# Optimization experiments

Measured on AMD Instinct MI355X. Metric: run time of the kernel, lower is better.

The kernel has to match this reference:

```python
import jax, jax.numpy as jnp
import numpy as np

B_, L, DM, DS, DC, EX = 8, 1024, 256, 16, 4, 2
DI = EX * DM            # d_inner = 512
DTR = max(DM // 16, 1)  # dt_rank = 16


def setup_inputs() -> dict:
    key = jax.random.key(0)
    ks = jax.random.split(key, 16)
    s = lambda i, shape, sc=0.05: jax.random.normal(ks[i], shape, dtype=jnp.float32) * sc
    return {
        "state": jax.random.normal(ks[0], (B_, L, DM), dtype=jnp.float32),
        "in_proj_w": s(1, (2 * DI, DM)),
        "conv_w": s(2, (DI, DC)),
        "conv_b": s(3, (DI,)),
        "x_proj_w": s(4, (DTR + 2 * DS, DI)),
        "dt_proj_w": s(5, (DI, DTR), 0.5),
        "dt_proj_b": s(6, (DI,)),
        "A_log": jnp.log(jnp.broadcast_to(jnp.arange(1, DS + 1, dtype=jnp.float32), (DI, DS))),
        "D": jnp.ones((DI,), jnp.float32),
        "out_proj_w": s(7, (DM, DI)),
        "w1": s(8, (DM, 256)), "b1": jnp.zeros((256,), jnp.float32),
        "w2": s(9, (256, 128)), "b2": jnp.zeros((128,), jnp.float32),
        "w3": s(10, (128, 1)), "b3": jnp.zeros((1,), jnp.float32),
    }


def reference(state, in_proj_w, conv_w, conv_b, x_proj_w, dt_proj_w, dt_proj_b,
              A_log, D, out_proj_w, w1, b1, w2, b2, w3, b3):
    # --- Mamba block ---
    xz = jnp.einsum('bld,ed->ble', state, in_proj_w)      # (B, L, 2*DI)
    x, z = jnp.split(xz, 2, axis=-1)
    # causal depthwise conv1d (kernel DC), small unrolled loop over taps
    xp = jnp.pad(x, ((0, 0), (DC - 1, 0), (0, 0)))
    xc = sum(xp[:, k:k + L, :] * conv_w[:, k] for k in range(DC)) + conv_b
    x = jax.nn.silu(xc)                                   # (B, L, DI)
    x_dbl = jnp.einsum('bld,ed->ble', x, x_proj_w)        # (B, L, DTR+2*DS)
    dtr, Bm, Cm = jnp.split(x_dbl, [DTR, DTR + DS], axis=-1)
    dt = jax.nn.softplus(jnp.einsum('blr,dr->bld', dtr, dt_proj_w) + dt_proj_b)
    A = -jnp.exp(A_log)                                   # (DI, DS)
    dA = jnp.exp(dt[..., None] * A)                       # (B, L, DI, DS)
    dBu = dt[..., None] * Bm[:, :, None, :] * x[..., None]

    def step(h, inp):
        dA_t, dBu_t, C_t = inp
        h = dA_t * h + dBu_t                              # (B, DI, DS)
        return h, jnp.einsum('bdn,bn->bd', h, C_t)

    h0 = jnp.zeros((x.shape[0], DI, DS), x.dtype)
    _, ys = jax.lax.scan(step, h0, (jnp.swapaxes(dA, 0, 1),
                                    jnp.swapaxes(dBu, 0, 1),
                                    jnp.swapaxes(Cm, 0, 1)))
    y = jnp.swapaxes(ys, 0, 1) + x * D                    # (B, L, DI)
    y = y * jax.nn.silu(z)
    out = jnp.einsum('bld,ed->ble', y, out_proj_w)        # (B, L, DM)
    # --- squeeze is a no-op for these shapes; MLP value head ---
    h1 = jax.nn.relu(out @ w1 + b1)
    h2 = jax.nn.relu(h1 @ w2 + b2)
    return h2 @ w3 + b3                                   # (B, L, 1)
```

## Files before the change

### kernel.cpp

```cpp
#include <hip/hip_runtime.h>
#include <cstdint>
#include <cmath>

#define B_   8
#define L_   1024
#define DM_  256
#define DS_  16
#define DC_  4
#define DI_  512
#define DTR_ 16
#define M_   (B_*L_)
#define NCH  64
#define CH   16

using half8 = __attribute__((ext_vector_type(8))) _Float16;
using half4 = __attribute__((ext_vector_type(4))) _Float16;
using f32x4 = __attribute__((ext_vector_type(4))) float;

template<bool F32>
__device__ __forceinline__ half8 load_h8(const void* base, size_t off)
{
    if constexpr (F32) {
        const float* p = (const float*)base + off;
        const float4 a = *reinterpret_cast<const float4*>(p);
        const float4 b = *reinterpret_cast<const float4*>(p + 4);
        half8 h;
        h[0] = (_Float16)a.x; h[1] = (_Float16)a.y;
        h[2] = (_Float16)a.z; h[3] = (_Float16)a.w;
        h[4] = (_Float16)b.x; h[5] = (_Float16)b.y;
        h[6] = (_Float16)b.z; h[7] = (_Float16)b.w;
        return h;
    } else {
        return *reinterpret_cast<const half8*>((const _Float16*)base + off);
    }
}

__global__ __launch_bounds__(256)
void prep_k(const float* __restrict__ state, const float* __restrict__ ipw,
            const float* __restrict__ opw,
            const float* __restrict__ w1, const float* __restrict__ w2,
            _Float16* __restrict__ st_h, _Float16* __restrict__ wih,
            _Float16* __restrict__ woh,
            _Float16* __restrict__ w1t, _Float16* __restrict__ w2t)
{
    const int g = blockIdx.x * 256 + threadIdx.x;
    const int N0 = M_ * DM_ / 4;
    const int N1 = N0 + 2 * DI_ * DM_ / 4;
    const int N2 = N1 + DM_ * DI_ / 4;
    const int N3 = N2 + 256 * 256;
    const int N4 = N3 + 256 * 128;
    if (g < N0) {
        const float4 v = reinterpret_cast<const float4*>(state)[g];
        half4 h; h[0]=(_Float16)v.x; h[1]=(_Float16)v.y; h[2]=(_Float16)v.z; h[3]=(_Float16)v.w;
        reinterpret_cast<half4*>(st_h)[g] = h;
    } else if (g < N1) {
        const int gg = g - N0;
        const float4 v = reinterpret_cast<const float4*>(ipw)[gg];
        half4 h; h[0]=(_Float16)v.x; h[1]=(_Float16)v.y; h[2]=(_Float16)v.z; h[3]=(_Float16)v.w;
        reinterpret_cast<half4*>(wih)[gg] = h;
    } else if (g < N2) {
        const int gg = g - N1;
        const float4 v = reinterpret_cast<const float4*>(opw)[gg];
        half4 h; h[0]=(_Float16)v.x; h[1]=(_Float16)v.y; h[2]=(_Float16)v.z; h[3]=(_Float16)v.w;
        reinterpret_cast<half4*>(woh)[gg] = h;
    } else if (g < N3) {
        const int gg = g - N2;
        const int r = gg >> 8, c = gg & 255;
        w1t[(size_t)c * 256 + r] = (_Float16)w1[gg];
    } else if (g < N4) {
        const int gg = g - N3;
        const int r = gg >> 7, c = gg & 127;
        w2t[(size_t)c * 256 + r] = (_Float16)w2[gg];
    }
}

__global__ __launch_bounds__(256)
void inproj_k(const _Float16* __restrict__ A, const _Float16* __restrict__ W,
              const float* __restrict__ cw, const float* __restrict__ cb,
              _Float16* __restrict__ xs, _Float16* __restrict__ gout)
{
    __shared__ _Float16 Ash[144][72];
    __shared__ _Float16 Bsh[64][72];
    _Float16 (*xsh)[152] = reinterpret_cast<_Float16(*)[152]>(&Ash[0][0]);

    const int tid  = threadIdx.x;
    const int lane = tid & 63;
    const int w    = tid >> 6;
    const int wm   = (w >> 1) * 64;
    const int wn   = (w & 1) * 32;
    const int bm   = blockIdx.x * 128;
    const int bn   = blockIdx.y * 64;
    const bool xside = (bn < DI_);
    const bool first = ((bm & (L_ - 1)) == 0);

    const int fr = lane & 15;
    const int fk = (lane >> 4) * 8;
    const int sr = tid >> 2;
    const int sc = (tid & 3) * 16;

    f32x4 acc[4][2] = {};
    f32x4 hacc[2] = {};

    for (int k0 = 0; k0 < DM_; k0 += 64) {
        #pragma unroll
        for (int hh = 0; hh < 2; hh++) {
            const int c = sc + hh * 8;
            *reinterpret_cast<half8*>(&Ash[16 + sr][c]) =
                *reinterpret_cast<const half8*>(A + (size_t)(bm + sr) * DM_ + k0 + c);
            *reinterpret_cast<half8*>(&Ash[16 + sr + 64][c]) =
                *reinterpret_cast<const half8*>(A + (size_t)(bm + sr + 64) * DM_ + k0 + c);
            *reinterpret_cast<half8*>(&Bsh[sr][c]) =
                *reinterpret_cast<const half8*>(W + (size_t)(bn + sr) * DM_ + k0 + c);
            if (tid < 64) {
                half8 hv = half8{};
                if (xside && !first)
                    hv = *reinterpret_cast<const half8*>(
                        A + (size_t)(bm - 16 + sr) * DM_ + k0 + c);
                *reinterpret_cast<half8*>(&Ash[sr][c]) = hv;
            }
        }
        __syncthreads();

        #pragma unroll
        for (int kk = 0; kk < 64; kk += 32) {
            half8 af[4], bf[2];
            #pragma unroll
            for (int mf = 0; mf < 4; mf++)
                af[mf] = *reinterpret_cast<const half8*>(&Ash[16 + wm + mf * 16 + fr][kk + fk]);
            #pragma unroll
            for (int nf = 0; nf < 2; nf++)
                bf[nf] = *reinterpret_cast<const half8*>(&Bsh[wn + nf * 16 + fr][kk + fk]);
            #pragma unroll
            for (int mf = 0; mf < 4; mf++)
                #pragma unroll
                for (int nf = 0; nf < 2; nf++)
                    acc[mf][nf] = __builtin_amdgcn_mfma_f32_16x16x32_f16(
                        af[mf], bf[nf], acc[mf][nf], 0, 0, 0);
            if (xside && w < 2) {
                const half8 ha = *reinterpret_cast<const half8*>(&Ash[fr][kk + fk]);
                #pragma unroll
                for (int nf = 0; nf < 2; nf++)
                    hacc[nf] = __builtin_amdgcn_mfma_f32_16x16x32_f16(
                        ha, bf[nf], hacc[nf], 0, 0, 0);
            }
        }
        __syncthreads();
    }

    const int orow = (lane >> 4) * 4;
    const int ocol = lane & 15;

    if (!xside) {
        #pragma unroll
        for (int mf = 0; mf < 4; mf++) {
            #pragma unroll
            for (int nf = 0; nf < 2; nf++) {
                const int gc = bn + wn + nf * 16 + ocol - DI_;
                #pragma unroll
                for (int r = 0; r < 4; r++) {
                    const int gr = bm + wm + mf * 16 + orow + r;
                    const float v = acc[mf][nf][r];
                    const float g = v * (1.f / (1.f + __expf(-v)));
                    gout[(size_t)gr * DI_ + gc] = (_Float16)g;
                }
            }
        }
        return;
    }

    #pragma unroll
    for (int mf = 0; mf < 4; mf++) {
        #pragma unroll
        for (int nf = 0; nf < 2; nf++) {
            half4 hv;
            #pragma unroll
            for (int r = 0; r < 4; r++) hv[r] = (_Float16)acc[mf][nf][r];
            *reinterpret_cast<half4*>(
                &xsh[wn + nf * 16 + ocol][16 + wm + mf * 16 + orow]) = hv;
        }
    }
    if (w < 2) {
        #pragma unroll
        for (int nf = 0; nf < 2; nf++) {
            half4 hv;
            #pragma unroll
            for (int r = 0; r < 4; r++) hv[r] = (_Float16)hacc[nf][r];
            *reinterpret_cast<half4*>(&xsh[wn + nf * 16 + ocol][orow]) = hv;
        }
    }
    __syncthreads();

    const int cc = tid & 63;
    const int r0 = (tid >> 6) * 32;
    const int gc = bn + cc;
    const float cb0 = cb[gc];
    float cwv[DC_];
    #pragma unroll
    for (int k = 0; k < DC_; k++) cwv[k] = cw[gc * DC_ + k];

    float xw[36];
    #pragma unroll
    for (int q = 0; q < 9; q++) {
        const half4 hv = *reinterpret_cast<const half4*>(&xsh[cc][12 + r0 + 4 * q]);
        #pragma unroll
        for (int j = 0; j < 4; j++) xw[4 * q + j] = (float)hv[j];
    }
    #pragma unroll
    for (int i = 0; i < 32; i++) {
        float a = cb0;
        #pragma unroll
        for (int k = 0; k < DC_; k++)
            a += xw[1 + i + k] * cwv[k];
        const float s = a * (1.f / (1.f + __expf(-a)));
        xs[(size_t)(bm + r0 + i) * DI_ + gc] = (_Float16)s;
    }
}

template<int ACT, bool BIAS>
__global__ __launch_bounds__(256)
void hgemm64_k(const _Float16* __restrict__ A, int lda,
               const _Float16* __restrict__ W,
               const float* __restrict__ bias,
               _Float16* __restrict__ Cv, int ldc, int K)
{
    __shared__ _Float16 Ash[64][40];
    __shared__ _Float16 Bsh[64][40];
    const int tid  = threadIdx.x;
    const int lane = tid & 63;
    const int w    = tid >> 6;
    const int wm   = (w >> 1) * 32;
    const int wn   = (w & 1) * 32;
    const int bm   = blockIdx.x * 64;
    const int bn   = blockIdx.y * 64;

    const int fr = lane & 15;
    const int fk = (lane >> 4) * 8;
    const int sr = tid >> 2;
    const int sg = (tid & 3) * 8;

    f32x4 acc[2][2] = {};

    for (int k0 = 0; k0 < K; k0 += 32) {
        *reinterpret_cast<half8*>(&Ash[sr][sg]) =
            load_h8<false>(A, (size_t)(bm + sr) * lda + k0 + sg);
        *reinterpret_cast<half8*>(&Bsh[sr][sg]) =
            load_h8<false>(W, (size_t)(bn + sr) * K + k0 + sg);
        __syncthreads();

        half8 af[2], bf[2];
        #pragma unroll
        for (int mf = 0; mf < 2; mf++)
            af[mf] = *reinterpret_cast<const half8*>(&Ash[wm + mf * 16 + fr][fk]);
        #pragma unroll
        for (int nf = 0; nf < 2; nf++)
            bf[nf] = *reinterpret_cast<const half8*>(&Bsh[wn + nf * 16 + fr][fk]);
        #pragma unroll
        for (int mf = 0; mf < 2; mf++)
            #pragma unroll
            for (int nf = 0; nf < 2; nf++)
                acc[mf][nf] = __builtin_amdgcn_mfma_f32_16x16x32_f16(
                    af[mf], bf[nf], acc[mf][nf], 0, 0, 0);
        __syncthreads();
    }

    const int orow = (lane >> 4) * 4;
    const int ocol = lane & 15;
    #pragma unroll
    for (int mf = 0; mf < 2; mf++) {
        #pragma unroll
        for (int nf = 0; nf < 2; nf++) {
            const int gc = bn + wn + nf * 16 + ocol;
            float b = BIAS ? bias[gc] : 0.f;
            #pragma unroll
            for (int r = 0; r < 4; r++) {
                const int gr = bm + wm + mf * 16 + orow + r;
                float v = acc[mf][nf][r] + b;
                if (ACT == 1) v = fmaxf(v, 0.f);
                Cv[(size_t)gr * ldc + gc] = (_Float16)v;
            }
        }
    }
}

__global__ __launch_bounds__(256)
void tail_k(const _Float16* __restrict__ h1, const _Float16* __restrict__ w2t,
            const float* __restrict__ b2, const float* __restrict__ w3,
            const float* __restrict__ b3, float* __restrict__ out)
{
    __shared__ _Float16 Ash[64][40];
    __shared__ _Float16 Bsh[128][40];
    __shared__ float red[64][2];
    const int tid  = threadIdx.x;
    const int lane = tid & 63;
    const int w    = tid >> 6;
    const int wm   = (w >> 1) * 32;
    const int wn   = (w & 1) * 64;
    const int bm   = blockIdx.x * 64;

    const int fr = lane & 15;
    const int fk = (lane >> 4) * 8;
    const int sr = tid >> 2;
    const int sg = (tid & 3) * 8;

    f32x4 acc[2][4] = {};

    for (int k0 = 0; k0 < 256; k0 += 32) {
        *reinterpret_cast<half8*>(&Ash[sr][sg]) =
            *reinterpret_cast<const half8*>(h1 + (size_t)(bm + sr) * 256 + k0 + sg);
        *reinterpret_cast<half8*>(&Bsh[sr][sg]) =
            *reinterpret_cast<const half8*>(w2t + (size_t)sr * 256 + k0 + sg);
        *reinterpret_cast<half8*>(&Bsh[sr + 64][sg]) =
            *reinterpret_cast<const half8*>(w2t + (size_t)(sr + 64) * 256 + k0 + sg);
        __syncthreads();

        half8 af[2], bf[4];
        #pragma unroll
        for (int mf = 0; mf < 2; mf++)
            af[mf] = *reinterpret_cast<const half8*>(&Ash[wm + mf * 16 + fr][fk]);
        #pragma unroll
        for (int nf = 0; nf < 4; nf++)
            bf[nf] = *reinterpret_cast<const half8*>(&Bsh[wn + nf * 16 + fr][fk]);
        #pragma unroll
        for (int mf = 0; mf < 2; mf++)
            #pragma unroll
            for (int nf = 0; nf < 4; nf++)
                acc[mf][nf] = __builtin_amdgcn_mfma_f32_16x16x32_f16(
                    af[mf], bf[nf], acc[mf][nf], 0, 0, 0);
        __syncthreads();
    }

    const int orow = (lane >> 4) * 4;
    const int ocol = lane & 15;
    float part[2][4];
    #pragma unroll
    for (int mf = 0; mf < 2; mf++) {
        #pragma unroll
        for (int r = 0; r < 4; r++) {
            float s = 0.f;
            #pragma unroll
            for (int nf = 0; nf < 4; nf++) {
                const int gc = wn + nf * 16 + ocol;
                float v = acc[mf][nf][r] + b2[gc];
                v = fmaxf(v, 0.f);
                s += v * w3[gc];
            }
            part[mf][r] = s;
        }
    }
    #pragma unroll
    for (int m = 1; m < 16; m <<= 1) {
        #pragma unroll
        for (int mf = 0; mf < 2; mf++)
            #pragma unroll
            for (int r = 0; r < 4; r++)
                part[mf][r] += __shfl_xor(part[mf][r], m);
    }
    if (ocol == 0) {
        #pragma unroll
        for (int mf = 0; mf < 2; mf++)
            #pragma unroll
            for (int r = 0; r < 4; r++)
                red[wm + mf * 16 + orow + r][w & 1] = part[mf][r];
    }
    __syncthreads();
    if (tid < 64)
        out[bm + tid] = red[tid][0] + red[tid][1] + b3[0];
}

__global__ __launch_bounds__(256)
void xproj_k(const _Float16* __restrict__ xs,
             const float* __restrict__ xpw,
             float* __restrict__ dtr32,
             float* __restrict__ xdbl32)
{
    __shared__ _Float16 Ash[64][40];
    __shared__ _Float16 Bsh[48][40];
    const int tid  = threadIdx.x;
    const int lane = tid & 63;
    const int w    = tid >> 6;
    const int bm   = blockIdx.x * 64;
    const int fr   = lane & 15;
    const int fk   = (lane >> 4) * 8;
    const int sr   = tid >> 2;
    const int sg   = (tid & 3) * 8;

    f32x4 acc[3] = {};

    for (int k0 = 0; k0 < 512; k0 += 32) {
        *reinterpret_cast<half8*>(&Ash[sr][sg]) =
            load_h8<false>(xs, (size_t)(bm + sr) * 512 + k0 + sg);
        if (sr < 48)
            *reinterpret_cast<half8*>(&Bsh[sr][sg]) =
                load_h8<true>(xpw, (size_t)sr * 512 + k0 + sg);
        __syncthreads();
        const half8 af = *reinterpret_cast<const half8*>(&Ash[w * 16 + fr][fk]);
        #pragma unroll
        for (int nf = 0; nf < 3; nf++) {
            const half8 bf = *reinterpret_cast<const half8*>(&Bsh[nf * 16 + fr][fk]);
            acc[nf] = __builtin_amdgcn_mfma_f32_16x16x32_f16(af, bf, acc[nf], 0, 0, 0);
        }
        __syncthreads();
    }

    const int orow = (lane >> 4) * 4;
    const int ocol = lane & 15;
    #pragma unroll
    for (int nf = 0; nf < 3; nf++) {
        #pragma unroll
        for (int r = 0; r < 4; r++) {
            const int gr = bm + w * 16 + orow + r;
            const float v = acc[nf][r];
            if (nf == 0)
                dtr32[(size_t)gr * 16 + ocol] = v;
            else
                xdbl32[(size_t)gr * 32 + (nf - 1) * 16 + ocol] = v;
        }
    }
}

__device__ __forceinline__ bool a_is_arange(const float* Av)
{
    bool fast = true;
    #pragma unroll
    for (int n = 1; n < DS_; n++)
        fast = fast && (fabsf(Av[n] - (n + 1) * Av[0]) <= 1e-3f * (n + 1));
    return fast;
}

__device__ __forceinline__ float dt_inline(const float* __restrict__ dr,
                                           const float* wreg, float bd)
{
    float v = bd;
    #pragma unroll
    for (int r = 0; r < DTR_; r++) v += dr[r] * wreg[r];
    return (v > 20.f) ? v : __logf(1.f + __expf(v));
}

__global__ __launch_bounds__(512)
void scan_phase1(const float* __restrict__ dtr32, const float* __restrict__ dtw,
                 const float* __restrict__ dtb, const _Float16* __restrict__ xs,
                 const float* __restrict__ xdbl32, const float* __restrict__ A_log,
                 _Float16* __restrict__ h_end, float* __restrict__ dtsum)
{
    const int c = blockIdx.x, b = blockIdx.y, d = threadIdx.x;
    float Av[DS_], wreg[DTR_];
    #pragma unroll
    for (int n = 0; n < DS_; n++) Av[n] = -expf(A_log[d * DS_ + n]);
    #pragma unroll
    for (int r = 0; r < DTR_; r++) wreg[r] = dtw[d * DTR_ + r];
    const float bd = dtb[d];
    float h[DS_] = {};
    float dts = 0.f;
    const int base = b * L_ + c * CH;
    const size_t rbase = (size_t)base * DI_ + d;
    if (a_is_arange(Av)) {
        const float Av0 = Av[0];
        #pragma unroll 4
        for (int tl = 0; tl < CH; tl++) {
            const float* dr = dtr32 + (size_t)(base + tl) * 16;
            const float* Br = xdbl32 + (size_t)(base + tl) * 32;
            const float dtv = dt_inline(dr, wreg, bd);
            const float xv  = (float)xs[rbase + (size_t)tl * DI_];
            dts += dtv;
            const float dtx = dtv * xv;
            const float e1 = __expf(dtv * Av0);
            float e = 1.f;
            #pragma unroll
            for (int n = 0; n < DS_; n++) {
                e *= e1;
                h[n] = e * h[n] + dtx * Br[n];
            }
        }
    } else {
        #pragma unroll 4
        for (int tl = 0; tl < CH; tl++) {
            const float* dr = dtr32 + (size_t)(base + tl) * 16;
            const float* Br = xdbl32 + (size_t)(base + tl) * 32;
            const float dtv = dt_inline(dr, wreg, bd);
            const float xv  = (float)xs[rbase + (size_t)tl * DI_];
            dts += dtv;
            const float dtx = dtv * xv;
            #pragma unroll
            for (int n = 0; n < DS_; n++)
                h[n] = __expf(dtv * Av[n]) * h[n] + dtx * Br[n];
        }
    }
    const size_t o = (size_t)(b * NCH + c) * DI_ + d;
    half8 v0, v1;
    #pragma unroll
    for (int n = 0; n < 8; n++) { v0[n] = (_Float16)h[n]; v1[n] = (_Float16)h[8 + n]; }
    half8* he = (half8*)(h_end + o * DS_);
    he[0] = v0; he[1] = v1;
    dtsum[o] = dts;
}

__global__ __launch_bounds__(256)
void scan_phase2(const _Float16* __restrict__ h_end, const float* __restrict__ dtsum,
                 const float* __restrict__ A_log, _Float16* __restrict__ h_start)
{
    const int gid = blockIdx.x * 256 + threadIdx.x;
    const int n = gid & 15;
    const int d = (gid >> 4) & (DI_ - 1);
    const int b = gid >> 13;
    const float Av = -expf(A_log[d * DS_ + n]);
    float hs = 0.f;
    #pragma unroll 8
    for (int c = 0; c < NCH; c++) {
        const size_t o = (size_t)(b * NCH + c) * DI_ + d;
        const float e  = __expf(Av * dtsum[o]);
        const float he = (float)h_end[o * DS_ + n];
        h_start[o * DS_ + n] = (_Float16)hs;
        hs = e * hs + he;
    }
}

__global__ __launch_bounds__(512)
void scan_phase3(const float* __restrict__ dtr32, const float* __restrict__ dtw,
                 const float* __restrict__ dtb, const _Float16* __restrict__ xs,
                 const float* __restrict__ xdbl32, const float* __restrict__ A_log,
                 const float* __restrict__ Dv, const _Float16* __restrict__ gbuf,
                 const _Float16* __restrict__ h_start, _Float16* __restrict__ yout)
{
    const int c = blockIdx.x, b = blockIdx.y, d = threadIdx.x;
    float Av[DS_], wreg[DTR_];
    #pragma unroll
    for (int n = 0; n < DS_; n++) Av[n] = -expf(A_log[d * DS_ + n]);
    #pragma unroll
    for (int r = 0; r < DTR_; r++) wreg[r] = dtw[d * DTR_ + r];
    const float bd = dtb[d];
    float h[DS_];
    {
        const half8* hsv = (const half8*)(h_start + ((size_t)(b * NCH + c) * DI_ + d) * DS_);
        const half8 a = hsv[0], bb = hsv[1];
        #pragma unroll
        for (int n = 0; n < 8; n++) { h[n] = (float)a[n]; h[8 + n] = (float)bb[n]; }
    }
    const float Dd = Dv[d];
    const int base = b * L_ + c * CH;
    const size_t rbase = (size_t)base * DI_ + d;
    if (a_is_arange(Av)) {
        const float Av0 = Av[0];
        #pragma unroll 4
        for (int tl = 0; tl < CH; tl++) {
            const float* dr = dtr32 + (size_t)(base + tl) * 16;
            const float* Br = xdbl32 + (size_t)(base + tl) * 32;
            const size_t off = rbase + (size_t)tl * DI_;
            const float dtv = dt_inline(dr, wreg, bd);
            const float xv  = (float)xs[off];
            const float g   = (float)gbuf[off];
            const float dtx = dtv * xv;
            const float e1 = __expf(dtv * Av0);
            float e = 1.f;
            float acc = 0.f;
            #pragma unroll
            for (int n = 0; n < DS_; n++) {
                e *= e1;
                h[n] = e * h[n] + dtx * Br[n];
                acc += h[n] * Br[16 + n];
            }
            const float yv = acc + xv * Dd;
            yout[off] = (_Float16)(yv * g);
        }
    } else {
        #pragma unroll 4
        for (int tl = 0; tl < CH; tl++) {
            const float* dr = dtr32 + (size_t)(base + tl) * 16;
            const float* Br = xdbl32 + (size_t)(base + tl) * 32;
            const size_t off = rbase + (size_t)tl * DI_;
            const float dtv = dt_inline(dr, wreg, bd);
            const float xv  = (float)xs[off];
            const float g   = (float)gbuf[off];
            const float dtx = dtv * xv;
            float acc = 0.f;
            #pragma unroll
            for (int n = 0; n < DS_; n++) {
                h[n] = __expf(dtv * Av[n]) * h[n] + dtx * Br[n];
                acc += h[n] * Br[16 + n];
            }
            const float yv = acc + xv * Dd;
            yout[off] = (_Float16)(yv * g);
        }
    }
}

extern "C" void kernel_launch(void* const* d_in, const int* in_sizes, int n_in,
                              void* d_out, int out_size, void* d_ws, size_t ws_size,
                              hipStream_t stream)
{
    const float* state      = (const float*)d_in[0];
    const float* in_proj_w  = (const float*)d_in[1];
    const float* conv_w     = (const float*)d_in[2];
    const float* conv_b     = (const float*)d_in[3];
    const float* x_proj_w   = (const float*)d_in[4];
    const float* dt_proj_w  = (const float*)d_in[5];
    const float* dt_proj_b  = (const float*)d_in[6];
    const float* A_log      = (const float*)d_in[7];
    const float* Dp         = (const float*)d_in[8];
    const float* out_proj_w = (const float*)d_in[9];
    const float* w1 = (const float*)d_in[10];
    const float* b1 = (const float*)d_in[11];
    const float* w2 = (const float*)d_in[12];
    const float* b2 = (const float*)d_in[13];
    const float* w3 = (const float*)d_in[14];
    const float* b3 = (const float*)d_in[15];

    float* ws = (float*)d_ws;
    float*    xdbl32 = ws;
    float*    dtr32  = xdbl32 + 262144;
    float*    dtsum  = dtr32 + 131072;
    _Float16* st_h   = (_Float16*)(dtsum + 262144);
    _Float16* wih    = st_h + 2097152;
    _Float16* woh    = wih + 262144;
    _Float16* gbuf   = woh + 131072;
    _Float16* xs_h   = gbuf + 4194304;
    _Float16* he_h   = xs_h + 4194304;
    _Float16* hs_h   = he_h + 4194304;
    _Float16* y_h    = hs_h + 4194304;
    _Float16* outb_h = y_h + 4194304;
    _Float16* h1_h   = outb_h + 2097152;
    _Float16* w1t    = h1_h + 2097152;
    _Float16* w2t    = w1t + 65536;

    prep_k<<<dim3(2816), 256, 0, stream>>>(
        state, in_proj_w, out_proj_w, w1, w2, st_h, wih, woh, w1t, w2t);

    inproj_k<<<dim3(M_/128, 1024/64), 256, 0, stream>>>(
        st_h, wih, conv_w, conv_b, xs_h, gbuf);
    xproj_k<<<dim3(M_/64), 256, 0, stream>>>(xs_h, x_proj_w, dtr32, xdbl32);
    scan_phase1<<<dim3(NCH, B_), 512, 0, stream>>>(
        dtr32, dt_proj_w, dt_proj_b, xs_h, xdbl32, A_log, he_h, dtsum);
    scan_phase2<<<dim3(256), 256, 0, stream>>>(he_h, dtsum, A_log, hs_h);
    scan_phase3<<<dim3(NCH, B_), 512, 0, stream>>>(
        dtr32, dt_proj_w, dt_proj_b, xs_h, xdbl32, A_log, Dp, gbuf, hs_h, y_h);
    hgemm64_k<0, false><<<dim3(M_/64, 256/64), 256, 0, stream>>>(
        y_h, DI_, woh, nullptr, outb_h, DM_, DI_);
    hgemm64_k<1, true><<<dim3(M_/64, 256/64), 256, 0, stream>>>(
        outb_h, DM_, w1t, b1, h1_h, 256, 256);
    tail_k<<<dim3(M_/64), 256, 0, stream>>>(h1_h, w2t, b2, w3, b3, (float*)d_out);
}
```

Before: 105.0 us.

## Fuse out_proj GEMM into scan phase 3 via LDS-staged y tile

Scan phase 3 now writes each chunk's gated y values (16 rows x 512) into shared memory instead of global memory. It then multiplies that tile by the out_proj weights with MFMA 16x16x32 f16 instructions and writes the 256-wide result directly. This removes the y buffer round trip through global memory and one kernel launch. In exchange, each block rereads the full out_proj weight matrix from global or L2 memory, and the small 16-row tile gives low MFMA reuse.

```diff
diff --git a/kernel.cpp b/kernel.cpp
--- a/kernel.cpp
+++ b/kernel.cpp
@@ -519,8 +519,10 @@
                  const float* __restrict__ dtb, const _Float16* __restrict__ xs,
                  const float* __restrict__ xdbl32, const float* __restrict__ A_log,
                  const float* __restrict__ Dv, const _Float16* __restrict__ gbuf,
-                 const _Float16* __restrict__ h_start, _Float16* __restrict__ yout)
-{
+                 const _Float16* __restrict__ h_start,
+                 const _Float16* __restrict__ woh, _Float16* __restrict__ outb)
+{
+    __shared__ _Float16 y_lds[CH][520];
     const int c = blockIdx.x, b = blockIdx.y, d = threadIdx.x;
     float Av[DS_], wreg[DTR_];
     #pragma unroll
@@ -559,7 +561,7 @@
                 acc += h[n] * Br[16 + n];
             }
             const float yv = acc + xv * Dd;
-            yout[off] = (_Float16)(yv * g);
+            y_lds[tl][d] = (_Float16)(yv * g);
         }
     } else {
         #pragma unroll 4
@@ -578,7 +580,35 @@
                 acc += h[n] * Br[16 + n];
             }
             const float yv = acc + xv * Dd;
-            yout[off] = (_Float16)(yv * g);
+            y_lds[tl][d] = (_Float16)(yv * g);
+        }
+    }
+    __syncthreads();
+
+    const int lane = threadIdx.x & 63;
+    const int w    = threadIdx.x >> 6;
+    const int fr   = lane & 15;
+    const int fk   = (lane >> 4) * 8;
+    f32x4 oacc[2] = {};
+    for (int k0 = 0; k0 < DI_; k0 += 32) {
+        const half8 af = *reinterpret_cast<const half8*>(&y_lds[fr][k0 + fk]);
+        #pragma unroll
+        for (int nt = 0; nt < 2; nt++) {
+            const int wr = (w * 2 + nt) * 16 + fr;
+            const half8 bf = *reinterpret_cast<const half8*>(
+                woh + (size_t)wr * DI_ + k0 + fk);
+            oacc[nt] = __builtin_amdgcn_mfma_f32_16x16x32_f16(af, bf, oacc[nt], 0, 0, 0);
+        }
+    }
+    const int orow = (lane >> 4) * 4;
+    const int ocol = lane & 15;
+    #pragma unroll
+    for (int nt = 0; nt < 2; nt++) {
+        const int gc = (w * 2 + nt) * 16 + ocol;
+        #pragma unroll
+        for (int r = 0; r < 4; r++) {
+            const int gr = base + orow + r;
+            outb[(size_t)gr * DM_ + gc] = (_Float16)oacc[nt][r];
         }
     }
 }
@@ -615,8 +645,7 @@
     _Float16* xs_h   = gbuf + 4194304;
     _Float16* he_h   = xs_h + 4194304;
     _Float16* hs_h   = he_h + 4194304;
-    _Float16* y_h    = hs_h + 4194304;
-    _Float16* outb_h = y_h + 4194304;
+    _Float16* outb_h = hs_h + 4194304;
     _Float16* h1_h   = outb_h + 2097152;
     _Float16* w1t    = h1_h + 2097152;
     _Float16* w2t    = w1t + 65536;
@@ -631,9 +660,8 @@
         dtr32, dt_proj_w, dt_proj_b, xs_h, xdbl32, A_log, he_h, dtsum);
     scan_phase2<<<dim3(256), 256, 0, stream>>>(he_h, dtsum, A_log, hs_h);
     scan_phase3<<<dim3(NCH, B_), 512, 0, stream>>>(
-        dtr32, dt_proj_w, dt_proj_b, xs_h, xdbl32, A_log, Dp, gbuf, hs_h, y_h);
-    hgemm64_k<0, false><<<dim3(M_/64, 256/64), 256, 0, stream>>>(
-        y_h, DI_, woh, nullptr, outb_h, DM_, DI_);
+        dtr32, dt_proj_w, dt_proj_b, xs_h, xdbl32, A_log, Dp, gbuf, hs_h,
+        woh, outb_h);
     hgemm64_k<1, true><<<dim3(M_/64, 256/64), 256, 0, stream>>>(
         outb_h, DM_, w1t, b1, h1_h, 256, 256);
     tail_k<<<dim3(M_/64), 256, 0, stream>>>(h1_h, w2t, b2, w3, b3, (float*)d_out);
```

After: 110.8 us. 5.5% more time.
